# Performance work log

Hardware: AMD Instinct MI355X
Metric: run time of the kernel (lower is better)

Reference implementation:

```python
import jax, jax.numpy as jnp
import numpy as np

DIM = 128
HEADS = 8
K_RATIO = 0.5
LAYER_SCALE = 0.1
EPS = 1e-6


def setup_inputs() -> dict:
    key = jax.random.key(0)
    ks = jax.random.split(key, 18)
    d = DIM
    hd3 = d * 3  # high-frequency channels (lh,hl,hh)
    f = lambda k, shape, s=0.05: jax.random.normal(k, shape, dtype=jnp.float32) * s
    return {
        "x": jax.random.normal(ks[0], (8, d, 64, 64), dtype=jnp.float32),
        "qkv_w": f(ks[1], (3 * d, d)),
        "proj_w": f(ks[2], (d, d)),
        "attn_gn_g": 1.0 + f(ks[3], (d,)),
        "attn_gn_b": f(ks[4], (d,)),
        "he_dw_w": f(ks[5], (hd3, 1, 3, 3)),
        "he_gn1_g": 1.0 + f(ks[6], (hd3,)),
        "he_gn1_b": f(ks[7], (hd3,)),
        "he_pw_w": f(ks[8], (hd3, hd3)),
        "he_gn2_g": 1.0 + f(ks[9], (hd3,)),
        "he_gn2_b": f(ks[10], (hd3,)),
        "alpha": jnp.array([0.1], dtype=jnp.float32),
        "ffn_w1": f(ks[11], (2 * d, d)),
        "ffn_gn1_g": 1.0 + f(ks[12], (2 * d,)),
        "ffn_gn1_b": f(ks[13], (2 * d,)),
        "ffn_w2": f(ks[14], (d, 2 * d)),
        "ffn_gn2_g": 1.0 + f(ks[15], (d,)),
        "ffn_gn2_b": f(ks[16], (d,)),
    }


def _group_norm(x, g, b, groups):
    B, C, H, W = x.shape
    xg = x.reshape(B, groups, -1)
    mu = xg.mean(-1, keepdims=True)
    var = xg.var(-1, keepdims=True)
    xn = ((xg - mu) * jax.lax.rsqrt(var + EPS)).reshape(B, C, H, W)
    return xn * g[:, None, None] + b[:, None, None]


def _conv1x1(x, w):
    return jnp.einsum('oc,bchw->bohw', w, x)


def _l2norm(t):
    # matches F.normalize(dim=-1, eps=1e-12): x / norm.clamp_min(eps)
    return t / jnp.maximum(jnp.linalg.norm(t, axis=-1, keepdims=True), 1e-12)


def _sparse_attn(ll, qkv_w, proj_w, g, b):
    B, C, H, W = ll.shape
    N = H * W
    nh = HEADS
    hd = C // nh
    scale = hd ** -0.5
    qkv = _conv1x1(ll, qkv_w).reshape(B, 3, nh, hd, N)
    q = jnp.swapaxes(qkv[:, 0], -1, -2)  # [B,nh,N,hd]
    k = jnp.swapaxes(qkv[:, 1], -1, -2)
    v = jnp.swapaxes(qkv[:, 2], -1, -2)
    q = _l2norm(q)
    k = _l2norm(k)
    attn = jnp.einsum('bhnd,bhmd->bhnm', q, k) * scale  # [B,nh,N,N]
    attn = jnp.clip(attn, -32.0, 32.0)  # fp32 clamp value
    k_num = max(int(N * K_RATIO), 1)
    if k_num < N:
        _, idx = jax.lax.top_k(attn, k_num)  # [B,nh,N,k_num]
        flat_attn = attn.reshape(-1, N)
        rows = jnp.arange(flat_attn.shape[0])[:, None]
        mask = jnp.zeros(flat_attn.shape, dtype=bool).at[rows, idx.reshape(-1, k_num)].set(True)
        attn = jnp.where(mask.reshape(attn.shape), attn, jnp.float32(-1e9))
    attn = jax.nn.softmax(attn, axis=-1)
    out = jnp.einsum('bhnm,bhmd->bhnd', attn, v)
    out = jnp.swapaxes(out, 2, 3).reshape(B, C, H, W)
    out = _conv1x1(out, proj_w)
    return _group_norm(out, g, b, min(32, C // 4))


def _high_enhance(h, dw_w, g1, b1, pw_w, g2, b2, alpha):
    C = h.shape[1]
    groups = min(32, C // 8)
    y = jax.lax.conv_general_dilated(
        h, dw_w, window_strides=(1, 1), padding='SAME',
        feature_group_count=C, dimension_numbers=('NCHW', 'OIHW', 'NCHW'))
    y = jax.nn.silu(_group_norm(y, g1, b1, groups))
    y = _group_norm(_conv1x1(y, pw_w), g2, b2, groups)
    return h + alpha[0] * y


def _iwt(ll, lh, hl, hh):
    a = ll - lh - hl + hh  # goes to (even row, even col)
    bq = ll - lh + hl - hh  # (odd row, even col)
    c = ll + lh - hl - hh  # (even row, odd col)
    d = ll + lh + hl + hh  # (odd row, odd col)
    B, C, H, W = ll.shape
    row_even = jnp.stack([a, c], axis=-1)  # [B,C,H,W,2] col parity
    row_odd = jnp.stack([bq, d], axis=-1)
    h = jnp.stack([row_even, row_odd], axis=3)  # [B,C,H,2,W,2]
    return h.reshape(B, C, 2 * H, 2 * W)


def _ffn(x, w1, g1, b1, w2, g2, b2):
    d = x.shape[1]
    groups = min(32, d // 4)
    y = _group_norm(_conv1x1(x, w1), g1, b1, groups)
    y = jax.nn.gelu(y, approximate=False)
    return _group_norm(_conv1x1(y, w2), g2, b2, groups)


def reference(x, qkv_w, proj_w, attn_gn_g, attn_gn_b,
              he_dw_w, he_gn1_g, he_gn1_b, he_pw_w, he_gn2_g, he_gn2_b, alpha,
              ffn_w1, ffn_gn1_g, ffn_gn1_b, ffn_w2, ffn_gn2_g, ffn_gn2_b):
    # DWT (Haar, stride-2 slicing)
    x1 = x[:, :, 0::2, 0::2]
    x2 = x[:, :, 1::2, 0::2]
    x3 = x[:, :, 0::2, 1::2]
    x4 = x[:, :, 1::2, 1::2]
    ll = (x1 + x2 + x3 + x4) * 0.5
    lh = (-x1 - x2 + x3 + x4) * 0.5
    hl = (-x1 + x2 - x3 + x4) * 0.5
    hh = (x1 - x2 - x3 + x4) * 0.5
    high = jnp.concatenate([lh, hl, hh], axis=1)

    ll_out = _sparse_attn(ll, qkv_w, proj_w, attn_gn_g, attn_gn_b)
    high_out = _high_enhance(high, he_dw_w, he_gn1_g, he_gn1_b, he_pw_w, he_gn2_g, he_gn2_b, alpha)

    C = ll.shape[1]
    x_rec = _iwt(ll + ll_out, high_out[:, :C], high_out[:, C:2 * C], high_out[:, 2 * C:])

    out = x + LAYER_SCALE * x_rec
    out = out + LAYER_SCALE * _ffn(out, ffn_w1, ffn_gn1_g, ffn_gn1_b, ffn_w2, ffn_gn2_g, ffn_gn2_b)
    return out
```

## Files before the change

### kernel.cpp

```cpp
#include <hip/hip_runtime.h>
#include <cstdint>
#include <cstddef>

#define BB 8
#define CC 128
#define C3 384
#define HH 64
#define H2 32
#define NPIX 1024
#define N4 4096
#define NHD 8
#define HD 16

typedef _Float16 h2f __attribute__((ext_vector_type(2)));
typedef _Float16 h4f __attribute__((ext_vector_type(4)));
typedef float f4 __attribute__((ext_vector_type(4)));

union U4H { uint4 u; h2f h[4]; };
union H4U { h4f v; h2f h[2]; };

__device__ inline h2f pkrtz(float a, float b) {
  return __builtin_bit_cast(h2f, __builtin_amdgcn_cvt_pkrtz(a, b));
}

__global__ __launch_bounds__(256) void k_dwt(const float* __restrict__ x,
                                             float* __restrict__ ll,
                                             float* __restrict__ high) {
  int idx = blockIdx.x * 256 + threadIdx.x;
  int w = idx & 31, h = (idx >> 5) & 31, c = (idx >> 10) & 127, b = idx >> 17;
  const float* xp = x + ((size_t)(b * CC + c) * HH + 2 * h) * HH + 2 * w;
  float x1 = xp[0];
  float x2 = xp[HH];
  float x3 = xp[1];
  float x4 = xp[HH + 1];
  int n = h * H2 + w;
  ll[(size_t)(b * CC + c) * NPIX + n]              = 0.5f * ( x1 + x2 + x3 + x4);
  high[((size_t)b * C3 + c) * NPIX + n]            = 0.5f * (-x1 - x2 + x3 + x4);
  high[((size_t)b * C3 + CC + c) * NPIX + n]       = 0.5f * (-x1 + x2 - x3 + x4);
  high[((size_t)b * C3 + 2 * CC + c) * NPIX + n]   = 0.5f * ( x1 - x2 - x3 + x4);
}

template <int CIN, int P, int OPT>
__global__ __launch_bounds__(256) void k_conv1x1(const float* __restrict__ in,
                                                 const float* __restrict__ w,
                                                 float* __restrict__ out,
                                                 int Cout, int Npix) {
  int tid = threadIdx.x;
  int n0 = (blockIdx.x * 256 + tid) * P;
  int o0 = blockIdx.y * OPT;
  int b = blockIdx.z;
  const float* inb = in + (size_t)b * CIN * Npix + n0;
  const float* wb = w + (size_t)o0 * CIN;
  float acc[OPT][P];
#pragma unroll
  for (int o = 0; o < OPT; ++o)
#pragma unroll
    for (int p = 0; p < P; ++p) acc[o][p] = 0.f;

  for (int c0 = 0; c0 < CIN; c0 += 8) {
#pragma unroll
    for (int c = 0; c < 8; ++c) {
      float vv[P];
      const float* ip = inb + (size_t)(c0 + c) * Npix;
      if constexpr (P == 4) {
        float4 t = *(const float4*)ip;
        vv[0] = t.x; vv[1] = t.y; vv[2] = t.z; vv[3] = t.w;
      } else if constexpr (P == 2) {
        float2 t = *(const float2*)ip;
        vv[0] = t.x; vv[1] = t.y;
      } else {
        vv[0] = ip[0];
      }
#pragma unroll
      for (int o = 0; o < OPT; ++o) {
        float wc = wb[(size_t)o * CIN + c0 + c];
#pragma unroll
        for (int p = 0; p < P; ++p) acc[o][p] = fmaf(wc, vv[p], acc[o][p]);
      }
    }
  }
  size_t ob = ((size_t)b * Cout + o0) * Npix + n0;
#pragma unroll
  for (int o = 0; o < OPT; ++o) {
    float* op = out + ob + (size_t)o * Npix;
    if constexpr (P == 4) {
      *(float4*)op = make_float4(acc[o][0], acc[o][1], acc[o][2], acc[o][3]);
    } else if constexpr (P == 2) {
      *(float2*)op = make_float2(acc[o][0], acc[o][1]);
    } else {
      op[0] = acc[o][0];
    }
  }
}

__global__ __launch_bounds__(256) void k_qkvnorm(const float* __restrict__ qkv,
                                                 uint4* __restrict__ qh,
                                                 uint4* __restrict__ kh,
                                                 uint16_t* __restrict__ vt) {
  __shared__ uint16_t lds_v[16 * 256];
  int tid = threadIdx.x;
  int idx = blockIdx.x * 256 + tid;
  int n = idx & 1023, h = (idx >> 10) & 7, b = idx >> 13;
  const float* base = qkv + ((size_t)b * C3 + h * HD) * NPIX + n;
  float q[HD], k[HD], vv[HD];
  float sq = 0.f, sk = 0.f;
#pragma unroll
  for (int d = 0; d < HD; ++d) {
    q[d] = base[(size_t)d * NPIX];
    k[d] = base[(size_t)(CC + d) * NPIX];
    vv[d] = base[(size_t)(2 * CC + d) * NPIX];
    sq += q[d] * q[d];
    sk += k[d] * k[d];
  }
  float rq = 1.f / fmaxf(sqrtf(sq), 1e-12f);
  float rk = 1.f / fmaxf(sqrtf(sk), 1e-12f);
#pragma unroll
  for (int g = 0; g < 2; ++g) {
    U4H pq, pk;
#pragma unroll
    for (int d = 0; d < 4; ++d) {
      int e = g * 8 + 2 * d;
      pq.h[d] = pkrtz(q[e] * rq, q[e + 1] * rq);
      pk.h[d] = pkrtz(k[e] * rk, k[e + 1] * rk);
    }
    qh[(size_t)idx * 2 + g] = pq.u;
    kh[(size_t)idx * 2 + g] = pk.u;
  }
#pragma unroll
  for (int d = 0; d < HD; ++d) {
    union { _Float16 f; uint16_t u; } cv;
    cv.f = (_Float16)vv[d];
    lds_v[d * 256 + tid] = cv.u;
  }
  __syncthreads();
  int bh = idx >> 10;
  int n0 = (blockIdx.x * 256) & 1023;
  const uint32_t* ldw = (const uint32_t*)lds_v;
  uint32_t* vtw = (uint32_t*)(vt + (size_t)bh * 16384 + n0);
#pragma unroll
  for (int r = 0; r < 8; ++r) {
    int d = 2 * r + (tid >> 7);
    int c = tid & 127;
    vtw[(size_t)d * 512 + c] = ldw[d * 128 + c];
  }
}

__global__ __launch_bounds__(256) void k_attn(const uint16_t* __restrict__ qh,
                                              const uint16_t* __restrict__ kh,
                                              const uint16_t* __restrict__ vt,
                                              float* __restrict__ attn_out) {
  int tid = threadIdx.x;
  int lane = tid & 63;
  int wave = tid >> 6;
  int blk = blockIdx.x;
  int bh = blk >> 4;
  int q0 = ((blk & 15) << 6) | (wave << 4);
  int lm = lane & 15;
  int lg = lane >> 4;
  int b = bh >> 3, h = bh & 7;

  H4U bq;
  bq.v = *(const h4f*)(qh + ((size_t)bh * 1024 + q0 + lm) * 16 + 4 * lg);
  const h2f qsc = {(_Float16)0.25f, (_Float16)0.25f};
  bq.h[0] *= qsc;
  bq.h[1] *= qsc;

  const f4 z = {0.f, 0.f, 0.f, 0.f};
  const uint16_t* kbase = kh + (size_t)bh * 16384 + 4 * lg;
  h2f sc[64][2];
#pragma unroll
  for (int j = 0; j < 64; ++j) {
    h4f ak = *(const h4f*)(kbase + (size_t)(16 * j + lm) * 16);
    f4 d = __builtin_amdgcn_mfma_f32_16x16x16f16(ak, bq.v, z, 0, 0, 0);
    sc[j][0] = pkrtz(d[0], d[1]);
    sc[j][1] = pkrtz(d[2], d[3]);
  }

  float lo = -0.26f, hi = 0.26f;
  _Float16 hlo = (_Float16)(-0.26f);
#pragma unroll 1
  for (int it = 0; it < 12; ++it) {
    float mid = 0.5f * (lo + hi);
    _Float16 hm = (_Float16)mid;
    int cc[4] = {0, 0, 0, 0};
#pragma unroll
    for (int j = 0; j < 64; ++j) {
      int a = 0;
      a += (sc[j][0][0] >= hm);
      a += (sc[j][0][1] >= hm);
      a += (sc[j][1][0] >= hm);
      a += (sc[j][1][1] >= hm);
      cc[j & 3] += a;
    }
    int c = (cc[0] + cc[1]) + (cc[2] + cc[3]);
    c += __shfl_xor(c, 16);
    c += __shfl_xor(c, 32);
    bool ge = (c >= 512);
    lo = ge ? mid : lo;
    hlo = ge ? hm : hlo;
    hi = ge ? hi : mid;
  }

  float ss[2] = {0.f, 0.f};
#pragma unroll
  for (int j = 0; j < 64; ++j) {
#pragma unroll
    for (int r = 0; r < 2; ++r) {
      h2f t = sc[j][r];
      float p0 = (t[0] >= hlo) ? __expf((float)t[0]) : 0.f;
      float p1 = (t[1] >= hlo) ? __expf((float)t[1]) : 0.f;
      ss[r] += p0 + p1;
      sc[j][r] = pkrtz(p0, p1);
    }
  }
  float sum = ss[0] + ss[1];
  sum += __shfl_xor(sum, 16);
  sum += __shfl_xor(sum, 32);
  float inv = 1.f / sum;

  const uint16_t* vbase = vt + (size_t)bh * 16384 + (size_t)lm * 1024 + 4 * lg;
  f4 acc[4] = {z, z, z, z};
#pragma unroll
  for (int j = 0; j < 64; ++j) {
    h4f va = *(const h4f*)(vbase + 16 * j);
    H4U pf;
    pf.h[0] = sc[j][0];
    pf.h[1] = sc[j][1];
    acc[j & 3] = __builtin_amdgcn_mfma_f32_16x16x16f16(va, pf.v, acc[j & 3], 0, 0, 0);
  }
  f4 o = (acc[0] + acc[1]) + (acc[2] + acc[3]);
#pragma unroll
  for (int e = 0; e < 4; ++e) {
    int dim = 4 * lg + e;
    attn_out[((size_t)(b * CC + h * HD + dim) * NPIX) + q0 + lm] = o[e] * inv;
  }
}

__global__ __launch_bounds__(256) void k_dwconv(const float* __restrict__ in,
                                                const float* __restrict__ w,
                                                float* __restrict__ out) {
  int n = blockIdx.x * 256 + threadIdx.x;
  int c = blockIdx.y, b = blockIdx.z;
  int i = n >> 5, j = n & 31;
  const float* inb = in + ((size_t)b * C3 + c) * NPIX;
  const float* wc = w + c * 9;
  float acc = 0.f;
#pragma unroll
  for (int di = -1; di <= 1; ++di) {
    int ii = i + di;
    if (ii < 0 || ii > 31) continue;
#pragma unroll
    for (int dj = -1; dj <= 1; ++dj) {
      int jj = j + dj;
      if (jj < 0 || jj > 31) continue;
      acc += inb[ii * 32 + jj] * wc[(di + 1) * 3 + (dj + 1)];
    }
  }
  out[((size_t)b * C3 + c) * NPIX + n] = acc;
}

template <int ACT, bool HAS_RES>
__global__ __launch_bounds__(512) void k_gn(const float* __restrict__ x,
                                            const float* __restrict__ res,
                                            float* __restrict__ out,
                                            const float* __restrict__ gamma,
                                            const float* __restrict__ beta,
                                            const float* __restrict__ alpha_ptr,
                                            float alpha_const,
                                            int chPerGroup, int Npix, int nshift) {
  int g = blockIdx.x & 31, b = blockIdx.x >> 5;
  int Cout = 32 * chPerGroup;
  int elems = chPerGroup * Npix;
  int nv = elems >> 2;
  size_t base = ((size_t)b * Cout + g * chPerGroup) * Npix;
  const float4* xv = (const float4*)(x + base);
  int tid = threadIdx.x;
  float s = 0.f, s2 = 0.f;
  for (int i = tid; i < nv; i += 512) {
    float4 v = xv[i];
    s += v.x + v.y + v.z + v.w;
    s2 += v.x * v.x + v.y * v.y + v.z * v.z + v.w * v.w;
  }
#pragma unroll
  for (int off = 32; off > 0; off >>= 1) {
    s += __shfl_xor(s, off);
    s2 += __shfl_xor(s2, off);
  }
  __shared__ float ls[8], ls2[8];
  int wv = tid >> 6, ln = tid & 63;
  if (ln == 0) { ls[wv] = s; ls2[wv] = s2; }
  __syncthreads();
  float st = 0.f, s2t = 0.f;
#pragma unroll
  for (int i = 0; i < 8; ++i) { st += ls[i]; s2t += ls2[i]; }
  float inv_n = 1.f / (float)elems;
  float mean = st * inv_n;
  float var = s2t * inv_n - mean * mean;
  float rstd = rsqrtf(var + 1e-6f);
  float a = alpha_ptr ? alpha_ptr[0] : alpha_const;
  const float4* rv = (const float4*)(res + base);
  float4* ov = (float4*)(out + base);
  int cshift = nshift - 2;
  for (int i = tid; i < nv; i += 512) {
    float4 v = xv[i];
    int cc = g * chPerGroup + (i >> cshift);
    float gm = gamma[cc], bt = beta[cc];
    float r[4] = {v.x, v.y, v.z, v.w};
#pragma unroll
    for (int p = 0; p < 4; ++p) {
      float gnv = (r[p] - mean) * rstd * gm + bt;
      if (ACT == 1)      r[p] = gnv / (1.f + __expf(-gnv));
      else if (ACT == 2) r[p] = 0.5f * gnv * (1.f + erff(gnv * 0.70710678118654752f));
      else               r[p] = gnv;
    }
    float4 o;
    if (HAS_RES) {
      float4 rr = rv[i];
      o = make_float4(rr.x + a * r[0], rr.y + a * r[1], rr.z + a * r[2], rr.w + a * r[3]);
    } else {
      o = make_float4(r[0], r[1], r[2], r[3]);
    }
    ov[i] = o;
  }
}

__global__ __launch_bounds__(256) void k_iwt(const float* __restrict__ x,
                                             const float* __restrict__ s1,
                                             const float* __restrict__ hout,
                                             float* __restrict__ out) {
  int idx = blockIdx.x * 256 + threadIdx.x;
  int w = idx & 31, h = (idx >> 5) & 31, c = (idx >> 10) & 127, b = idx >> 17;
  int n = h * 32 + w;
  float ll = s1[(size_t)(b * CC + c) * NPIX + n];
  float lh = hout[((size_t)b * C3 + c) * NPIX + n];
  float hl = hout[((size_t)b * C3 + CC + c) * NPIX + n];
  float hh = hout[((size_t)b * C3 + 2 * CC + c) * NPIX + n];
  float va = ll - lh - hl + hh;
  float vb = ll - lh + hl - hh;
  float vc = ll + lh - hl - hh;
  float vd = ll + lh + hl + hh;
  size_t xb = ((size_t)(b * CC + c) * HH + 2 * h) * HH + 2 * w;
  out[xb]          = x[xb]          + 0.1f * va;
  out[xb + 1]      = x[xb + 1]      + 0.1f * vc;
  out[xb + HH]     = x[xb + HH]     + 0.1f * vb;
  out[xb + HH + 1] = x[xb + HH + 1] + 0.1f * vd;
}

extern "C" void kernel_launch(void* const* d_in, const int* in_sizes, int n_in,
                              void* d_out, int out_size, void* d_ws, size_t ws_size,
                              hipStream_t stream) {
  const float* x         = (const float*)d_in[0];
  const float* qkv_w     = (const float*)d_in[1];
  const float* proj_w    = (const float*)d_in[2];
  const float* attn_gn_g = (const float*)d_in[3];
  const float* attn_gn_b = (const float*)d_in[4];
  const float* he_dw_w   = (const float*)d_in[5];
  const float* he_gn1_g  = (const float*)d_in[6];
  const float* he_gn1_b  = (const float*)d_in[7];
  const float* he_pw_w   = (const float*)d_in[8];
  const float* he_gn2_g  = (const float*)d_in[9];
  const float* he_gn2_b  = (const float*)d_in[10];
  const float* alpha     = (const float*)d_in[11];
  const float* ffn_w1    = (const float*)d_in[12];
  const float* ffn_gn1_g = (const float*)d_in[13];
  const float* ffn_gn1_b = (const float*)d_in[14];
  const float* ffn_w2    = (const float*)d_in[15];
  const float* ffn_gn2_g = (const float*)d_in[16];
  const float* ffn_gn2_b = (const float*)d_in[17];
  float* out = (float*)d_out;

  float* ws = (float*)d_ws;
  float* ll   = ws;
  float* high = ws + 1048576;
  float* qkv  = ws + 4194304;
  float* qnkv = ws + 7340032;
  float* atto = ws + 10485760;
  float* proj = ws + 11534336;
  float* f1   = ws + 12582912;
  float* f3   = ws + 20971520;
  uint4* qh = (uint4*)qnkv;
  uint4* kh = (uint4*)(qnkv + 524288);
  uint16_t* vt = (uint16_t*)(qnkv + 1048576);
  float* y1 = qkv;
  float* pw = qnkv;

  k_dwt<<<4096, 256, 0, stream>>>(x, ll, high);
  k_conv1x1<128, 1, 8><<<dim3(4, 48, 8), 256, 0, stream>>>(ll, qkv_w, qkv, 384, 1024);
  k_qkvnorm<<<256, 256, 0, stream>>>(qkv, qh, kh, vt);
  k_attn<<<1024, 256, 0, stream>>>((const uint16_t*)qh, (const uint16_t*)kh, vt, atto);
  k_conv1x1<128, 1, 4><<<dim3(4, 32, 8), 256, 0, stream>>>(atto, proj_w, proj, 128, 1024);
  k_gn<0, true><<<256, 512, 0, stream>>>(proj, ll, proj, attn_gn_g, attn_gn_b,
                                         nullptr, 1.0f, 4, 1024, 10);
  k_dwconv<<<dim3(4, 384, 8), 256, 0, stream>>>(high, he_dw_w, y1);
  k_gn<1, false><<<256, 512, 0, stream>>>(y1, nullptr, y1, he_gn1_g, he_gn1_b,
                                          nullptr, 0.f, 12, 1024, 10);
  k_conv1x1<384, 1, 8><<<dim3(4, 48, 8), 256, 0, stream>>>(y1, he_pw_w, pw, 384, 1024);
  k_gn<0, true><<<256, 512, 0, stream>>>(pw, high, pw, he_gn2_g, he_gn2_b,
                                         alpha, 0.f, 12, 1024, 10);
  k_iwt<<<4096, 256, 0, stream>>>(x, proj, pw, out);
  k_conv1x1<128, 2, 8><<<dim3(8, 32, 8), 256, 0, stream>>>(out, ffn_w1, f1, 256, 4096);
  k_gn<2, false><<<256, 512, 0, stream>>>(f1, nullptr, f1, ffn_gn1_g, ffn_gn1_b,
                                          nullptr, 0.f, 8, 4096, 12);
  k_conv1x1<256, 2, 8><<<dim3(8, 16, 8), 256, 0, stream>>>(f1, ffn_w2, f3, 128, 4096);
  k_gn<0, true><<<256, 512, 0, stream>>>(f3, out, out, ffn_gn2_g, ffn_gn2_b,
                                         nullptr, 0.1f, 4, 4096, 12);
  (void)in_sizes; (void)n_in; (void)out_size; (void)ws_size;
}
```

Measured before the change: 416.6 us.

## Split attention key range across four waves with LDS-reduced threshold search

```diff
diff --git a/kernel.cpp b/kernel.cpp
--- a/kernel.cpp
+++ b/kernel.cpp
@@ -149,12 +149,15 @@
                                               const uint16_t* __restrict__ kh,
                                               const uint16_t* __restrict__ vt,
                                               float* __restrict__ attn_out) {
+  __shared__ int cnt_lds[12 * 64];
+  __shared__ float sum_lds[64];
+  __shared__ f4 obuf[4 * 64];
   int tid = threadIdx.x;
   int lane = tid & 63;
-  int wave = tid >> 6;
+  int w = tid >> 6;
   int blk = blockIdx.x;
-  int bh = blk >> 4;
-  int q0 = ((blk & 15) << 6) | (wave << 4);
+  int bh = blk >> 6;
+  int q0 = (blk & 63) << 4;
   int lm = lane & 15;
   int lg = lane >> 4;
   int b = bh >> 3, h = bh & 7;
@@ -167,10 +170,11 @@
 
   const f4 z = {0.f, 0.f, 0.f, 0.f};
   const uint16_t* kbase = kh + (size_t)bh * 16384 + 4 * lg;
-  h2f sc[64][2];
-#pragma unroll
-  for (int j = 0; j < 64; ++j) {
-    h4f ak = *(const h4f*)(kbase + (size_t)(16 * j + lm) * 16);
+  h2f sc[16][2];
+#pragma unroll
+  for (int j = 0; j < 16; ++j) {
+    int J = (w << 4) | j;
+    h4f ak = *(const h4f*)(kbase + (size_t)(16 * J + lm) * 16);
     f4 d = __builtin_amdgcn_mfma_f32_16x16x16f16(ak, bq.v, z, 0, 0, 0);
     sc[j][0] = pkrtz(d[0], d[1]);
     sc[j][1] = pkrtz(d[2], d[3]);
@@ -182,57 +186,66 @@
   for (int it = 0; it < 12; ++it) {
     float mid = 0.5f * (lo + hi);
     _Float16 hm = (_Float16)mid;
-    int cc[4] = {0, 0, 0, 0};
-#pragma unroll
-    for (int j = 0; j < 64; ++j) {
-      int a = 0;
-      a += (sc[j][0][0] >= hm);
-      a += (sc[j][0][1] >= hm);
-      a += (sc[j][1][0] >= hm);
-      a += (sc[j][1][1] >= hm);
-      cc[j & 3] += a;
-    }
-    int c = (cc[0] + cc[1]) + (cc[2] + cc[3]);
+    int c = 0;
+#pragma unroll
+    for (int j = 0; j < 16; ++j) {
+      c += (sc[j][0][0] >= hm);
+      c += (sc[j][0][1] >= hm);
+      c += (sc[j][1][0] >= hm);
+      c += (sc[j][1][1] >= hm);
+    }
     c += __shfl_xor(c, 16);
     c += __shfl_xor(c, 32);
-    bool ge = (c >= 512);
+    if (lg == 0) cnt_lds[it * 64 + lm * 4 + w] = c;
+    __syncthreads();
+    int4 c4 = *(const int4*)&cnt_lds[it * 64 + lm * 4];
+    int ct = (c4.x + c4.y) + (c4.z + c4.w);
+    bool ge = (ct >= 512);
     lo = ge ? mid : lo;
     hlo = ge ? hm : hlo;
     hi = ge ? hi : mid;
   }
 
-  float ss[2] = {0.f, 0.f};
-#pragma unroll
-  for (int j = 0; j < 64; ++j) {
+  float ss = 0.f;
+#pragma unroll
+  for (int j = 0; j < 16; ++j) {
 #pragma unroll
     for (int r = 0; r < 2; ++r) {
       h2f t = sc[j][r];
       float p0 = (t[0] >= hlo) ? __expf((float)t[0]) : 0.f;
       float p1 = (t[1] >= hlo) ? __expf((float)t[1]) : 0.f;
-      ss[r] += p0 + p1;
+      ss += p0 + p1;
       sc[j][r] = pkrtz(p0, p1);
     }
   }
-  float sum = ss[0] + ss[1];
-  sum += __shfl_xor(sum, 16);
-  sum += __shfl_xor(sum, 32);
-  float inv = 1.f / sum;
+  ss += __shfl_xor(ss, 16);
+  ss += __shfl_xor(ss, 32);
+  if (lg == 0) sum_lds[lm * 4 + w] = ss;
+  __syncthreads();
+  float4 s4 = *(const float4*)&sum_lds[lm * 4];
+  float inv = 1.f / ((s4.x + s4.y) + (s4.z + s4.w));
 
   const uint16_t* vbase = vt + (size_t)bh * 16384 + (size_t)lm * 1024 + 4 * lg;
-  f4 acc[4] = {z, z, z, z};
-#pragma unroll
-  for (int j = 0; j < 64; ++j) {
-    h4f va = *(const h4f*)(vbase + 16 * j);
+  f4 acc[2] = {z, z};
+#pragma unroll
+  for (int j = 0; j < 16; ++j) {
+    int J = (w << 4) | j;
+    h4f va = *(const h4f*)(vbase + 16 * J);
     H4U pf;
     pf.h[0] = sc[j][0];
     pf.h[1] = sc[j][1];
-    acc[j & 3] = __builtin_amdgcn_mfma_f32_16x16x16f16(va, pf.v, acc[j & 3], 0, 0, 0);
-  }
-  f4 o = (acc[0] + acc[1]) + (acc[2] + acc[3]);
-#pragma unroll
-  for (int e = 0; e < 4; ++e) {
-    int dim = 4 * lg + e;
-    attn_out[((size_t)(b * CC + h * HD + dim) * NPIX) + q0 + lm] = o[e] * inv;
+    acc[j & 1] = __builtin_amdgcn_mfma_f32_16x16x16f16(va, pf.v, acc[j & 1], 0, 0, 0);
+  }
+  f4 o = acc[0] + acc[1];
+  obuf[(w << 6) | lane] = o;
+  __syncthreads();
+  if (w == 0) {
+    f4 t = obuf[lane] + obuf[64 + lane] + obuf[128 + lane] + obuf[192 + lane];
+#pragma unroll
+    for (int e = 0; e < 4; ++e) {
+      int dim = 4 * lg + e;
+      attn_out[((size_t)(b * CC + h * HD + dim) * NPIX) + q0 + lm] = t[e] * inv;
+    }
   }
 }
 
@@ -387,7 +400,7 @@
   k_dwt<<<4096, 256, 0, stream>>>(x, ll, high);
   k_conv1x1<128, 1, 8><<<dim3(4, 48, 8), 256, 0, stream>>>(ll, qkv_w, qkv, 384, 1024);
   k_qkvnorm<<<256, 256, 0, stream>>>(qkv, qh, kh, vt);
-  k_attn<<<1024, 256, 0, stream>>>((const uint16_t*)qh, (const uint16_t*)kh, vt, atto);
+  k_attn<<<4096, 256, 0, stream>>>((const uint16_t*)qh, (const uint16_t*)kh, vt, atto);
   k_conv1x1<128, 1, 4><<<dim3(4, 32, 8), 256, 0, stream>>>(atto, proj_w, proj, 128, 1024);
   k_gn<0, true><<<256, 512, 0, stream>>>(proj, ll, proj, attn_gn_g, attn_gn_b,
                                          nullptr, 1.0f, 4, 1024, 10);
```

Measured after the change: 398.5 us. -4.3%, faster.
